# Performance work log

Measured on AMD Instinct MI355X. Metric: run time of the kernel, lower is better.

The kernel has to match this reference:

```python
import jax, jax.numpy as jnp
import numpy as np

DIM = 1024
NUM_HEADS = 16
HEAD_DIM = DIM // NUM_HEADS
SCALE = HEAD_DIM ** -0.5


def setup_inputs() -> dict:
    key = jax.random.key(0)
    k1, k2, k3 = jax.random.split(key, 3)
    B, S = 2, 2048
    x = jax.random.normal(k1, (B, S, DIM), dtype=jnp.float32)
    # nn.Linear(dim, 3*dim, bias=False): store as [in, out] for x @ W
    w_qkv = jax.random.normal(k2, (DIM, 3 * DIM), dtype=jnp.float32) * (DIM ** -0.5)
    w_out = jax.random.normal(k3, (DIM, DIM), dtype=jnp.float32) * (DIM ** -0.5)
    return {"x": x, "w_qkv": w_qkv, "w_out": w_out}


def reference(x, w_qkv, w_out):
    B, S, _ = x.shape
    qkv = x @ w_qkv                               # [B,S,3*D]
    q, k, v = jnp.split(qkv, 3, axis=-1)          # each [B,S,D]
    def heads(t):
        return t.reshape(B, S, NUM_HEADS, HEAD_DIM).transpose(0, 2, 1, 3)  # [B,H,S,d]
    q, k, v = heads(q), heads(k), heads(v)
    scores = jnp.einsum('bhqd,bhkd->bhqk', q, k) * SCALE   # [B,H,S,S]
    probs = jax.nn.softmax(scores, axis=-1)
    out = jnp.einsum('bhqk,bhkd->bhqd', probs, v)          # [B,H,S,d]
    out = out.transpose(0, 2, 1, 3).reshape(B, S, DIM)
    return out @ w_out
```

## Files before the change

kernel.cpp:

```cpp
#include <hip/hip_runtime.h>


typedef __bf16 bf16x8 __attribute__((ext_vector_type(8)));
typedef __bf16 bf16x4 __attribute__((ext_vector_type(4)));
typedef float floatx4 __attribute__((ext_vector_type(4)));

#define MFMA16(a, b, c) __builtin_amdgcn_mfma_f32_16x16x32_bf16((a), (b), (c), 0, 0, 0)

#if defined(__has_builtin)
#if __has_builtin(__builtin_amdgcn_exp2f)
#define EXP2F __builtin_amdgcn_exp2f
#endif
#endif
#ifndef EXP2F
#define EXP2F exp2f
#endif

__device__ __forceinline__ unsigned pk_bf16(float a, float b) {
  unsigned r;
  asm("v_cvt_pk_bf16_f32 %0, %1, %2" : "=v"(r) : "v"(a), "v"(b));
  return r;
}

__device__ __forceinline__ void gl_lds16(const void* g, void* l) {
  __builtin_amdgcn_global_load_lds((__attribute__((address_space(1))) void*)(g),
                                   (__attribute__((address_space(3))) void*)(l),
                                   16, 0, 0);
}

__global__ __launch_bounds__(256) void prep(const float* __restrict__ x,
                                            const float* __restrict__ w_qkv,
                                            const float* __restrict__ w_out,
                                            __bf16* __restrict__ xb,
                                            __bf16* __restrict__ wqkvt,
                                            __bf16* __restrict__ woutt) {
  __shared__ float tile[64][65];
  const int bid = blockIdx.x, t = threadIdx.x;
  if (bid < 4096) {
    int i = (bid * 256 + t) * 4;
    float4 v = *(const float4*)(x + i);
    bf16x4 o = { (__bf16)v.x, (__bf16)v.y, (__bf16)v.z, (__bf16)v.w };
    *(bf16x4*)(xb + i) = o;
    return;
  }
  const float* w;
  __bf16* wt;
  int K = 1024, N, k0, n0;
  if (bid < 4864) {
    int i = bid - 4096;
    w = w_qkv; wt = wqkvt; N = 3072; k0 = (i & 15) * 64; n0 = (i >> 4) * 64;
  } else {
    int i = bid - 4864;
    w = w_out; wt = woutt; N = 1024; k0 = (i & 15) * 64; n0 = (i >> 4) * 64;
  }
  for (int j = 0; j < 16; ++j) {
    int e = j * 256 + t, r = e >> 6, c = e & 63;
    tile[r][c] = w[(size_t)(k0 + r) * N + n0 + c];
  }
  __syncthreads();
  for (int j = 0; j < 16; ++j) {
    int e = j * 256 + t, r = e >> 6, c = e & 63;
    wt[(size_t)(n0 + r) * K + k0 + c] = (__bf16)tile[c][r];
  }
}

__global__ __launch_bounds__(256) void gemm_qkv(const __bf16* __restrict__ A,
                                                const __bf16* __restrict__ Bt,
                                                __bf16* __restrict__ qkb,
                                                __bf16* __restrict__ vt) {
  constexpr int K = 1024;
  constexpr float QSCALE = 0.18033688f;
  __shared__ __align__(16) __bf16 aS[128 * 32];
  __shared__ __align__(16) __bf16 bS[128 * 32];
  const int t = threadIdx.x;
  const int lane = t & 63, wave = t >> 6;
  const int l15 = lane & 15, quad = lane >> 4;
  const int wm = wave >> 1, wn = wave & 1;
  const int m0 = blockIdx.y * 128, n0 = blockIdx.x * 128;

  const floatx4 fzero = {0.f, 0.f, 0.f, 0.f};
  floatx4 acc[4][4];
  for (int mt = 0; mt < 4; ++mt)
    for (int nt = 0; nt < 4; ++nt) acc[mt][nt] = fzero;

  const int arow = t >> 2;
  const int ach = ((t & 3) ^ (arow & 3)) * 8;
  const __bf16* gA0 = A + (size_t)(m0 + arow) * K + ach;
  const __bf16* gA1 = gA0 + (size_t)64 * K;
  const __bf16* gB0 = Bt + (size_t)(n0 + arow) * K + ach;
  const __bf16* gB1 = gB0 + (size_t)64 * K;
  const int swz = (quad ^ (l15 & 3)) * 8;

  for (int k0 = 0; k0 < K; k0 += 32) {
    __syncthreads();
    gl_lds16(gA0 + k0, (char*)aS + t * 16);
    gl_lds16(gA1 + k0, (char*)aS + 4096 + t * 16);
    gl_lds16(gB0 + k0, (char*)bS + t * 16);
    gl_lds16(gB1 + k0, (char*)bS + 4096 + t * 16);
    __syncthreads();

    bf16x8 af[4], bfr[4];
    for (int mt = 0; mt < 4; ++mt)
      af[mt] = *(const bf16x8*)(aS + (wm * 64 + mt * 16 + l15) * 32 + swz);
    for (int nt = 0; nt < 4; ++nt)
      bfr[nt] = *(const bf16x8*)(bS + (wn * 64 + nt * 16 + l15) * 32 + swz);
    for (int mt = 0; mt < 4; ++mt)
      for (int nt = 0; nt < 4; ++nt)
        acc[mt][nt] = MFMA16(af[mt], bfr[nt], acc[mt][nt]);
  }

  for (int mt = 0; mt < 4; ++mt) {
    int row = m0 + wm * 64 + mt * 16 + quad * 4;
    for (int nt = 0; nt < 4; ++nt) {
      int col0 = n0 + wn * 64 + nt * 16;
      if (col0 >= 2048) {
        int dfull = col0 + l15 - 2048;
        int bh = ((row >> 11) << 4) + (dfull >> 6);
        int d = dfull & 63, s0 = row & 2047;
        bf16x4 pk = { (__bf16)acc[mt][nt][0], (__bf16)acc[mt][nt][1],
                      (__bf16)acc[mt][nt][2], (__bf16)acc[mt][nt][3] };
        *(bf16x4*)(vt + ((size_t)bh * 64 + d) * 2048 + s0) = pk;
      } else {
        float sc = (col0 < 1024) ? QSCALE : 1.0f;
        int col = col0 + l15;
        __bf16* cp = qkb + (size_t)row * 2048 + col;
        for (int r = 0; r < 4; ++r) cp[(size_t)r * 2048] = (__bf16)(acc[mt][nt][r] * sc);
      }
    }
  }
}

__global__ __launch_bounds__(256) void gemm_n64(const __bf16* __restrict__ A,
                                                const __bf16* __restrict__ Bt,
                                                float* __restrict__ C) {
  constexpr int K = 1024, N = 1024;
  __shared__ __align__(16) __bf16 aS[128 * 32];
  __shared__ __align__(16) __bf16 bS[64 * 32];
  const int t = threadIdx.x;
  const int lane = t & 63, wave = t >> 6;
  const int l15 = lane & 15, quad = lane >> 4;
  const int m0 = blockIdx.y * 128, n0 = blockIdx.x * 64;

  const floatx4 fzero = {0.f, 0.f, 0.f, 0.f};
  floatx4 acc[2][4];
  for (int mt = 0; mt < 2; ++mt)
    for (int nt = 0; nt < 4; ++nt) acc[mt][nt] = fzero;

  const int arow = t >> 2;
  const int ach = ((t & 3) ^ (arow & 3)) * 8;
  const __bf16* gA0 = A + (size_t)(m0 + arow) * K + ach;
  const __bf16* gA1 = gA0 + (size_t)64 * K;
  const __bf16* gB0 = Bt + (size_t)(n0 + arow) * K + ach;
  const int swz = (quad ^ (l15 & 3)) * 8;

  for (int k0 = 0; k0 < K; k0 += 32) {
    __syncthreads();
    gl_lds16(gA0 + k0, (char*)aS + t * 16);
    gl_lds16(gA1 + k0, (char*)aS + 4096 + t * 16);
    gl_lds16(gB0 + k0, (char*)bS + t * 16);
    __syncthreads();

    bf16x8 af[2], bfr[4];
    for (int mt = 0; mt < 2; ++mt)
      af[mt] = *(const bf16x8*)(aS + (wave * 32 + mt * 16 + l15) * 32 + swz);
    for (int nt = 0; nt < 4; ++nt)
      bfr[nt] = *(const bf16x8*)(bS + (nt * 16 + l15) * 32 + swz);
    for (int mt = 0; mt < 2; ++mt)
      for (int nt = 0; nt < 4; ++nt)
        acc[mt][nt] = MFMA16(af[mt], bfr[nt], acc[mt][nt]);
  }

  for (int mt = 0; mt < 2; ++mt) {
    int row = m0 + wave * 32 + mt * 16 + quad * 4;
    for (int nt = 0; nt < 4; ++nt) {
      int col = n0 + nt * 16 + l15;
      float* cp = C + (size_t)row * N + col;
      for (int r = 0; r < 4; ++r) cp[(size_t)r * N] = acc[mt][nt][r];
    }
  }
}

__global__ __launch_bounds__(256, 2) void flash_attn(const __bf16* __restrict__ qkb,
                                                     const __bf16* __restrict__ vt,
                                                     __bf16* __restrict__ out) {
  __shared__ __align__(16) __bf16 kS[2 * 64 * 64];
  __shared__ __align__(16) __bf16 vS[2 * 64 * 64];

  const int t = threadIdx.x;
  const int lane = t & 63, wave = t >> 6;
  const int l15 = lane & 15, quad = lane >> 4;
  const int id = blockIdx.x;
  const int xcd = id & 7, slot = id >> 3;
  const int bh = xcd * 4 + (slot >> 4), qb = slot & 15;
  const int b = bh >> 4, h = bh & 15;

  bf16x8 qf[2][2];
  for (int qt = 0; qt < 2; ++qt) {
    const __bf16* qp = qkb +
        (size_t)(b * 2048 + qb * 128 + wave * 32 + qt * 16 + l15) * 2048 + h * 64 + quad * 8;
    qf[qt][0] = *(const bf16x8*)qp;
    qf[qt][1] = *(const bf16x8*)(qp + 32);
  }

  bf16x8 onef;
  for (int j = 0; j < 8; ++j) onef[j] = (__bf16)1.0f;

  const floatx4 fzero = {0.f, 0.f, 0.f, 0.f};
  floatx4 oacc[2][4], lacc[2];
  for (int qt = 0; qt < 2; ++qt) {
    lacc[qt] = fzero;
    for (int dt = 0; dt < 4; ++dt) oacc[qt][dt] = fzero;
  }

  const int srow = t >> 3, schk = (t & 7) ^ (srow & 7);
  const __bf16* kg0 =
      qkb + (size_t)(b * 2048 + srow) * 2048 + 1024 + h * 64 + schk * 8;
  const __bf16* kg1 = kg0 + (size_t)32 * 2048;
  const __bf16* vg0 =
      vt + (size_t)bh * 64 * 2048 + (size_t)srow * 2048 + schk * 8;
  const __bf16* vg1 = vg0 + (size_t)32 * 2048;

  const int l7 = l15 & 7;

  bf16x8 kf[4][2];
  bf16x8 vfA[2][4], vfB[2][4];
  floatx4 saA[2][4], saB[2][4];

  auto stage = [&](int tile) {
    const size_t n1 = (size_t)tile * 64;
    const int oB = (tile & 1) * 8192;
    gl_lds16(kg0 + n1 * 2048, (char*)kS + oB + t * 16);
    gl_lds16(kg1 + n1 * 2048, (char*)kS + oB + 4096 + t * 16);
    gl_lds16(vg0 + n1, (char*)vS + oB + t * 16);
    gl_lds16(vg1 + n1, (char*)vS + oB + 4096 + t * 16);
  };

  auto loadKV = [&](int buf, bf16x8 (&vf)[2][4]) {
    const __bf16* kC = kS + buf * 4096;
    const __bf16* vC = vS + buf * 4096;
    for (int nt = 0; nt < 4; ++nt)
      for (int ks = 0; ks < 2; ++ks)
        kf[nt][ks] = *(const bf16x8*)(kC + (nt * 16 + l15) * 64 +
                                      ((ks * 4 + quad) ^ l7) * 8);
    for (int ks = 0; ks < 2; ++ks)
      for (int dt = 0; dt < 4; ++dt)
        vf[ks][dt] = *(const bf16x8*)(vC + (dt * 16 + l15) * 64 +
                                      ((ks * 4 + quad) ^ l7) * 8);
  };

  auto qk = [&](floatx4 (&sa)[2][4]) {
    __builtin_amdgcn_s_setprio(1);
    for (int qt = 0; qt < 2; ++qt)
      for (int nt = 0; nt < 4; ++nt) {
        floatx4 a = fzero;
        a = MFMA16(kf[nt][0], qf[qt][0], a);
        a = MFMA16(kf[nt][1], qf[qt][1], a);
        sa[qt][nt] = a;
      }
    __builtin_amdgcn_s_setprio(0);
  };

  auto smpv = [&](floatx4 (&sa)[2][4], bf16x8 (&vf)[2][4]) {
    for (int qt = 0; qt < 2; ++qt) {
      bf16x8 pa[2];
      for (int ks = 0; ks < 2; ++ks) {
        const int n0 = 2 * ks, n1 = 2 * ks + 1;
        float e00 = EXP2F(sa[qt][n0][0]), e01 = EXP2F(sa[qt][n0][1]);
        float e02 = EXP2F(sa[qt][n0][2]), e03 = EXP2F(sa[qt][n0][3]);
        float e10 = EXP2F(sa[qt][n1][0]), e11 = EXP2F(sa[qt][n1][1]);
        float e12 = EXP2F(sa[qt][n1][2]), e13 = EXP2F(sa[qt][n1][3]);
        unsigned x0 = pk_bf16(e00, e01), x1 = pk_bf16(e02, e03);
        unsigned y0 = pk_bf16(e10, e11), y1 = pk_bf16(e12, e13);
        unsigned d0 = x0, d2 = y0;
        asm("v_permlane32_swap_b32 %0, %1" : "+v"(d0), "+v"(d2));
        asm("v_permlane16_swap_b32 %0, %1" : "+v"(d0), "+v"(d2));
        unsigned d1 = x1, d3 = y1;
        asm("v_permlane32_swap_b32 %0, %1" : "+v"(d1), "+v"(d3));
        asm("v_permlane16_swap_b32 %0, %1" : "+v"(d1), "+v"(d3));
        union { unsigned u[4]; bf16x8 v8; } pu;
        pu.u[0] = d0; pu.u[1] = d1; pu.u[2] = d2; pu.u[3] = d3;
        pa[ks] = pu.v8;
      }
      __builtin_amdgcn_s_setprio(1);
      for (int ks = 0; ks < 2; ++ks) {
        for (int dt = 0; dt < 4; ++dt)
          oacc[qt][dt] = MFMA16(pa[ks], vf[ks][dt], oacc[qt][dt]);
        lacc[qt] = MFMA16(pa[ks], onef, lacc[qt]);
      }
      __builtin_amdgcn_s_setprio(0);
    }
  };

  stage(0);
  __syncthreads();
  stage(1);
  loadKV(0, vfA);
  qk(saA);

  for (int nb = 1; nb < 31; nb += 2) {
    __syncthreads();
    stage(nb + 1);
    loadKV(1, vfB);
    smpv(saA, vfA);
    qk(saB);
    __syncthreads();
    stage(nb + 2);
    loadKV(0, vfA);
    smpv(saB, vfB);
    qk(saA);
  }

  __syncthreads();
  loadKV(1, vfB);
  smpv(saA, vfA);
  qk(saB);
  smpv(saB, vfB);

  for (int qt = 0; qt < 2; ++qt) {
    float inv[4];
    for (int r = 0; r < 4; ++r) inv[r] = 1.f / lacc[qt][r];
    __bf16* ob = out +
        (size_t)(b * 2048 + qb * 128 + wave * 32 + qt * 16 + quad * 4) * 1024 + h * 64;
    for (int dt = 0; dt < 4; ++dt)
      for (int r = 0; r < 4; ++r)
        ob[(size_t)r * 1024 + dt * 16 + l15] = (__bf16)(oacc[qt][dt][r] * inv[r]);
  }
}

extern "C" void kernel_launch(void* const* d_in, const int* in_sizes, int n_in,
                              void* d_out, int out_size, void* d_ws, size_t ws_size,
                              hipStream_t stream) {
  const float* x = (const float*)d_in[0];
  const float* w_qkv = (const float*)d_in[1];
  const float* w_out = (const float*)d_in[2];
  float* out = (float*)d_out;

  char* ws = (char*)d_ws;
  __bf16* xb = (__bf16*)(ws);
  __bf16* wqkvt = (__bf16*)(ws + ((size_t)8 << 20));
  __bf16* qkb = (__bf16*)(ws + ((size_t)16 << 20));
  __bf16* vtg = (__bf16*)(ws + ((size_t)32 << 20));
  __bf16* aout = (__bf16*)(ws + ((size_t)40 << 20));
  __bf16* woutt = (__bf16*)(ws + ((size_t)48 << 20));

  prep<<<5120, 256, 0, stream>>>(x, w_qkv, w_out, xb, wqkvt, woutt);
  gemm_qkv<<<dim3(24, 32), 256, 0, stream>>>(xb, wqkvt, qkb, vtg);
  flash_attn<<<512, 256, 0, stream>>>(qkb, vtg, aout);
  gemm_n64<<<dim3(16, 32), 256, 0, stream>>>(aout, woutt, out);
}
```

Measured before the change: 172.9 us.

## Rewrite QKV GEMM with 256x256 tiles, double-buffered LDS, and split-phase MFMA pipeline

The QKV projection GEMM moves from 128x128 tiles with 256 threads and a single LDS buffer to 256x256 tiles with 512 threads, a BK of 64, and double-buffered LDS. Global-to-LDS loads for the next k-step are issued while MFMAs run on the current buffer. Explicit vmcnt/lgkmcnt waits, s_setprio and sched barriers control the interleaving. This is meant to hide memory latency and improve data reuse, at the cost of 128KB of LDS per block, much higher register pressure (32 accumulators per thread), and only 192 blocks, which could leave some CUs idle.

Result: slower. 176.8 us (+2.2%).

```diff
diff --git a/kernel.cpp b/kernel.cpp
--- a/kernel.cpp
+++ b/kernel.cpp
@@ -64,70 +64,146 @@
   }
 }
 
-__global__ __launch_bounds__(256) void gemm_qkv(const __bf16* __restrict__ A,
-                                                const __bf16* __restrict__ Bt,
-                                                __bf16* __restrict__ qkb,
-                                                __bf16* __restrict__ vt) {
+__global__ __launch_bounds__(512, 2) void gemm_qkv(const __bf16* __restrict__ A,
+                                                   const __bf16* __restrict__ Bt,
+                                                   __bf16* __restrict__ qkb,
+                                                   __bf16* __restrict__ vt) {
   constexpr int K = 1024;
   constexpr float QSCALE = 0.18033688f;
-  __shared__ __align__(16) __bf16 aS[128 * 32];
-  __shared__ __align__(16) __bf16 bS[128 * 32];
+  __shared__ __align__(16) __bf16 aL[2][2][128 * 64];
+  __shared__ __align__(16) __bf16 bL[2][2][128 * 64];
   const int t = threadIdx.x;
   const int lane = t & 63, wave = t >> 6;
-  const int l15 = lane & 15, quad = lane >> 4;
-  const int wm = wave >> 1, wn = wave & 1;
-  const int m0 = blockIdx.y * 128, n0 = blockIdx.x * 128;
+  const int l15 = lane & 15, quad = lane >> 4, l7 = l15 & 7;
+  const int wr = wave >> 2, wc = wave & 3;
+  const int m0 = blockIdx.y * 256, n0 = blockIdx.x * 256;
 
   const floatx4 fzero = {0.f, 0.f, 0.f, 0.f};
-  floatx4 acc[4][4];
-  for (int mt = 0; mt < 4; ++mt)
-    for (int nt = 0; nt < 4; ++nt) acc[mt][nt] = fzero;
-
-  const int arow = t >> 2;
-  const int ach = ((t & 3) ^ (arow & 3)) * 8;
-  const __bf16* gA0 = A + (size_t)(m0 + arow) * K + ach;
-  const __bf16* gA1 = gA0 + (size_t)64 * K;
-  const __bf16* gB0 = Bt + (size_t)(n0 + arow) * K + ach;
-  const __bf16* gB1 = gB0 + (size_t)64 * K;
-  const int swz = (quad ^ (l15 & 3)) * 8;
-
-  for (int k0 = 0; k0 < K; k0 += 32) {
-    __syncthreads();
-    gl_lds16(gA0 + k0, (char*)aS + t * 16);
-    gl_lds16(gA1 + k0, (char*)aS + 4096 + t * 16);
-    gl_lds16(gB0 + k0, (char*)bS + t * 16);
-    gl_lds16(gB1 + k0, (char*)bS + 4096 + t * 16);
-    __syncthreads();
-
-    bf16x8 af[4], bfr[4];
-    for (int mt = 0; mt < 4; ++mt)
-      af[mt] = *(const bf16x8*)(aS + (wm * 64 + mt * 16 + l15) * 32 + swz);
-    for (int nt = 0; nt < 4; ++nt)
-      bfr[nt] = *(const bf16x8*)(bS + (wn * 64 + nt * 16 + l15) * 32 + swz);
-    for (int mt = 0; mt < 4; ++mt)
-      for (int nt = 0; nt < 4; ++nt)
-        acc[mt][nt] = MFMA16(af[mt], bfr[nt], acc[mt][nt]);
-  }
-
-  for (int mt = 0; mt < 4; ++mt) {
-    int row = m0 + wm * 64 + mt * 16 + quad * 4;
-    for (int nt = 0; nt < 4; ++nt) {
-      int col0 = n0 + wn * 64 + nt * 16;
+  floatx4 acc[8][4];
+#pragma unroll
+  for (int i = 0; i < 8; ++i)
+#pragma unroll
+    for (int j = 0; j < 4; ++j) acc[i][j] = fzero;
+
+  const int r0 = t >> 3;
+  const int c8 = ((t & 7) ^ (r0 & 7)) * 8;
+  const __bf16* gA = A + (size_t)(m0 + r0) * K + c8;
+  const __bf16* gB = Bt + (size_t)(n0 + r0) * K + c8;
+
+#define STAGE_A(buf, kofs)                                        \
+  do {                                                            \
+    char* d0 = (char*)aL[buf][0] + t * 16;                        \
+    char* d1 = (char*)aL[buf][1] + t * 16;                        \
+    gl_lds16(gA + (kofs), d0);                                    \
+    gl_lds16(gA + (size_t)64 * K + (kofs), d0 + 8192);            \
+    gl_lds16(gA + (size_t)128 * K + (kofs), d1);                  \
+    gl_lds16(gA + (size_t)192 * K + (kofs), d1 + 8192);           \
+  } while (0)
+
+#define STAGE_B(buf, kofs)                                        \
+  do {                                                            \
+    char* d0 = (char*)bL[buf][0] + t * 16;                        \
+    char* d1 = (char*)bL[buf][1] + t * 16;                        \
+    gl_lds16(gB + (kofs), d0);                                    \
+    gl_lds16(gB + (size_t)64 * K + (kofs), d0 + 8192);            \
+    gl_lds16(gB + (size_t)128 * K + (kofs), d1);                  \
+    gl_lds16(gB + (size_t)192 * K + (kofs), d1 + 8192);           \
+  } while (0)
+
+  bf16x8 af[4][2], bf[4][2];
+#define LOAD_B(buf)                                                       \
+  do {                                                                    \
+    const __bf16* base = bL[buf][wc >> 1] + (wc & 1) * 64 * 64;           \
+    _Pragma("unroll") for (int nf = 0; nf < 4; ++nf)                      \
+        _Pragma("unroll") for (int kk = 0; kk < 2; ++kk)                  \
+            bf[nf][kk] = *(const bf16x8*)(base + (nf * 16 + l15) * 64 +   \
+                                          ((kk * 4 + quad) ^ l7) * 8);    \
+  } while (0)
+
+#define LOAD_A(buf, mh)                                                   \
+  do {                                                                    \
+    const __bf16* base = aL[buf][wr] + (mh) * 64 * 64;                    \
+    _Pragma("unroll") for (int mf = 0; mf < 4; ++mf)                      \
+        _Pragma("unroll") for (int kk = 0; kk < 2; ++kk)                  \
+            af[mf][kk] = *(const bf16x8*)(base + (mf * 16 + l15) * 64 +   \
+                                          ((kk * 4 + quad) ^ l7) * 8);    \
+  } while (0)
+
+#define MFMA_PH(mh)                                                       \
+  do {                                                                    \
+    __builtin_amdgcn_s_setprio(1);                                        \
+    _Pragma("unroll") for (int mf = 0; mf < 4; ++mf)                      \
+        _Pragma("unroll") for (int nf = 0; nf < 4; ++nf) {                \
+      floatx4 c = acc[(mh) * 4 + mf][nf];                                 \
+      c = MFMA16(af[mf][0], bf[nf][0], c);                                \
+      c = MFMA16(af[mf][1], bf[nf][1], c);                                \
+      acc[(mh) * 4 + mf][nf] = c;                                         \
+    }                                                                     \
+    __builtin_amdgcn_s_setprio(0);                                        \
+  } while (0)
+
+#define VMCNT4 asm volatile("s_waitcnt vmcnt(4)" ::: "memory")
+#define VMCNT0 asm volatile("s_waitcnt vmcnt(0)" ::: "memory")
+#define LGKM0 asm volatile("s_waitcnt lgkmcnt(0)" ::: "memory")
+#define BAR asm volatile("s_barrier" ::: "memory")
+#define SCHED0 __builtin_amdgcn_sched_barrier(0)
+
+  STAGE_A(0, 0);
+  STAGE_B(0, 0);
+
+  for (int j = 0; j < 15; ++j) {
+    const int cb = j & 1, nb = cb ^ 1;
+    const int kn = (j + 1) * 64;
+    STAGE_A(nb, kn);
+    VMCNT4;
+    BAR;
+    LOAD_B(cb);
+    LOAD_A(cb, 0);
+    LGKM0; SCHED0;
+    MFMA_PH(0);
+    STAGE_B(nb, kn);
+    LOAD_A(cb, 1);
+    LGKM0; SCHED0;
+    MFMA_PH(1);
+    BAR;
+  }
+  VMCNT0;
+  BAR;
+  LOAD_B(1);
+  LOAD_A(1, 0);
+  LGKM0; SCHED0;
+  MFMA_PH(0);
+  LOAD_A(1, 1);
+  LGKM0; SCHED0;
+  MFMA_PH(1);
+
+#pragma unroll
+  for (int mf8 = 0; mf8 < 8; ++mf8) {
+    int row = m0 + wr * 128 + mf8 * 16 + quad * 4;
+#pragma unroll
+    for (int nf = 0; nf < 4; ++nf) {
+      int col0 = n0 + wc * 64 + nf * 16;
       if (col0 >= 2048) {
         int dfull = col0 + l15 - 2048;
         int bh = ((row >> 11) << 4) + (dfull >> 6);
         int d = dfull & 63, s0 = row & 2047;
-        bf16x4 pk = { (__bf16)acc[mt][nt][0], (__bf16)acc[mt][nt][1],
-                      (__bf16)acc[mt][nt][2], (__bf16)acc[mt][nt][3] };
+        bf16x4 pk = { (__bf16)acc[mf8][nf][0], (__bf16)acc[mf8][nf][1],
+                      (__bf16)acc[mf8][nf][2], (__bf16)acc[mf8][nf][3] };
         *(bf16x4*)(vt + ((size_t)bh * 64 + d) * 2048 + s0) = pk;
       } else {
         float sc = (col0 < 1024) ? QSCALE : 1.0f;
         int col = col0 + l15;
         __bf16* cp = qkb + (size_t)row * 2048 + col;
-        for (int r = 0; r < 4; ++r) cp[(size_t)r * 2048] = (__bf16)(acc[mt][nt][r] * sc);
+#pragma unroll
+        for (int r = 0; r < 4; ++r) cp[(size_t)r * 2048] = (__bf16)(acc[mf8][nf][r] * sc);
       }
     }
   }
+#undef STAGE_A
+#undef STAGE_B
+#undef LOAD_A
+#undef LOAD_B
+#undef MFMA_PH
 }
 
 __global__ __launch_bounds__(256) void gemm_n64(const __bf16* __restrict__ A,
@@ -344,7 +420,7 @@
   __bf16* woutt = (__bf16*)(ws + ((size_t)48 << 20));
 
   prep<<<5120, 256, 0, stream>>>(x, w_qkv, w_out, xb, wqkvt, woutt);
-  gemm_qkv<<<dim3(24, 32), 256, 0, stream>>>(xb, wqkvt, qkb, vtg);
+  gemm_qkv<<<dim3(12, 16), 512, 0, stream>>>(xb, wqkvt, qkb, vtg);
   flash_attn<<<512, 256, 0, stream>>>(qkb, vtg, aout);
   gemm_n64<<<dim3(16, 32), 256, 0, stream>>>(aout, woutt, out);
 }
```

## Double-buffer GEMM LDS tiles with BK=64 and async prefetch pipeline

Applied to the files above, without the earlier changes.

Both projection GEMMs now stage 64-wide K tiles into double-buffered LDS, issuing the next tile's global-to-LDS loads before computing on the current one. Explicit vmcnt waits and barriers replace the two syncthreads per step. The loads use an 8-way XOR swizzle, and MFMA sections get raised wave priority. This is meant to hide global load latency and halve barrier count, at the cost of more LDS per block (64KB/48KB), which may limit occupancy despite launch_bounds(256,2).

Measured after the change: 173.7 us. No clear change (+0.4%).

```diff
diff --git a/kernel.cpp b/kernel.cpp
--- a/kernel.cpp
+++ b/kernel.cpp
@@ -27,6 +27,11 @@
                                    (__attribute__((address_space(3))) void*)(l),
                                    16, 0, 0);
 }
+
+#define VMCNT(n) asm volatile("s_waitcnt vmcnt(" #n ")" ::: "memory")
+#define LGKM0 asm volatile("s_waitcnt lgkmcnt(0)" ::: "memory")
+#define SBAR __builtin_amdgcn_s_barrier()
+#define SCHED0 __builtin_amdgcn_sched_barrier(0)
 
 __global__ __launch_bounds__(256) void prep(const float* __restrict__ x,
                                             const float* __restrict__ w_qkv,
@@ -64,118 +69,203 @@
   }
 }
 
-__global__ __launch_bounds__(256) void gemm_qkv(const __bf16* __restrict__ A,
-                                                const __bf16* __restrict__ Bt,
-                                                __bf16* __restrict__ qkb,
-                                                __bf16* __restrict__ vt) {
+__global__ __launch_bounds__(256, 2) void gemm_qkv(const __bf16* __restrict__ A,
+                                                   const __bf16* __restrict__ Bt,
+                                                   __bf16* __restrict__ qkb,
+                                                   __bf16* __restrict__ vt) {
   constexpr int K = 1024;
   constexpr float QSCALE = 0.18033688f;
-  __shared__ __align__(16) __bf16 aS[128 * 32];
-  __shared__ __align__(16) __bf16 bS[128 * 32];
+  __shared__ __align__(16) __bf16 aL[2][128 * 64];
+  __shared__ __align__(16) __bf16 bL[2][128 * 64];
   const int t = threadIdx.x;
   const int lane = t & 63, wave = t >> 6;
-  const int l15 = lane & 15, quad = lane >> 4;
+  const int l15 = lane & 15, quad = lane >> 4, l7 = l15 & 7;
   const int wm = wave >> 1, wn = wave & 1;
   const int m0 = blockIdx.y * 128, n0 = blockIdx.x * 128;
 
   const floatx4 fzero = {0.f, 0.f, 0.f, 0.f};
   floatx4 acc[4][4];
-  for (int mt = 0; mt < 4; ++mt)
-    for (int nt = 0; nt < 4; ++nt) acc[mt][nt] = fzero;
-
-  const int arow = t >> 2;
-  const int ach = ((t & 3) ^ (arow & 3)) * 8;
-  const __bf16* gA0 = A + (size_t)(m0 + arow) * K + ach;
-  const __bf16* gA1 = gA0 + (size_t)64 * K;
-  const __bf16* gB0 = Bt + (size_t)(n0 + arow) * K + ach;
-  const __bf16* gB1 = gB0 + (size_t)64 * K;
-  const int swz = (quad ^ (l15 & 3)) * 8;
-
-  for (int k0 = 0; k0 < K; k0 += 32) {
-    __syncthreads();
-    gl_lds16(gA0 + k0, (char*)aS + t * 16);
-    gl_lds16(gA1 + k0, (char*)aS + 4096 + t * 16);
-    gl_lds16(gB0 + k0, (char*)bS + t * 16);
-    gl_lds16(gB1 + k0, (char*)bS + 4096 + t * 16);
-    __syncthreads();
-
-    bf16x8 af[4], bfr[4];
-    for (int mt = 0; mt < 4; ++mt)
-      af[mt] = *(const bf16x8*)(aS + (wm * 64 + mt * 16 + l15) * 32 + swz);
-    for (int nt = 0; nt < 4; ++nt)
-      bfr[nt] = *(const bf16x8*)(bS + (wn * 64 + nt * 16 + l15) * 32 + swz);
-    for (int mt = 0; mt < 4; ++mt)
-      for (int nt = 0; nt < 4; ++nt)
-        acc[mt][nt] = MFMA16(af[mt], bfr[nt], acc[mt][nt]);
-  }
-
-  for (int mt = 0; mt < 4; ++mt) {
-    int row = m0 + wm * 64 + mt * 16 + quad * 4;
-    for (int nt = 0; nt < 4; ++nt) {
-      int col0 = n0 + wn * 64 + nt * 16;
+#pragma unroll
+  for (int i = 0; i < 4; ++i)
+#pragma unroll
+    for (int j = 0; j < 4; ++j) acc[i][j] = fzero;
+
+  const int r0 = t >> 3;
+  const int c8 = ((t & 7) ^ (r0 & 7)) * 8;
+  const __bf16* gA = A + (size_t)(m0 + r0) * K + c8;
+  const __bf16* gB = Bt + (size_t)(n0 + r0) * K + c8;
+
+  auto stageAB = [&](int buf, int kofs) {
+    char* da = (char*)aL[buf] + t * 16;
+    char* db = (char*)bL[buf] + t * 16;
+#pragma unroll
+    for (int r = 0; r < 4; ++r) {
+      gl_lds16(gA + (size_t)(32 * r) * K + kofs, da + r * 4096);
+      gl_lds16(gB + (size_t)(32 * r) * K + kofs, db + r * 4096);
+    }
+  };
+
+  bf16x8 af[4][2], bfr[4][2];
+  auto loadAB = [&](int buf) {
+#pragma unroll
+    for (int mf = 0; mf < 4; ++mf)
+#pragma unroll
+      for (int kk = 0; kk < 2; ++kk)
+        af[mf][kk] = *(const bf16x8*)(aL[buf] + (wm * 64 + mf * 16 + l15) * 64 +
+                                      ((kk * 4 + quad) ^ l7) * 8);
+#pragma unroll
+    for (int nf = 0; nf < 4; ++nf)
+#pragma unroll
+      for (int kk = 0; kk < 2; ++kk)
+        bfr[nf][kk] = *(const bf16x8*)(bL[buf] + (wn * 64 + nf * 16 + l15) * 64 +
+                                       ((kk * 4 + quad) ^ l7) * 8);
+  };
+
+  auto mfmaAll = [&]() {
+    __builtin_amdgcn_s_setprio(1);
+#pragma unroll
+    for (int mf = 0; mf < 4; ++mf)
+#pragma unroll
+      for (int nf = 0; nf < 4; ++nf) {
+        floatx4 c = acc[mf][nf];
+        c = MFMA16(af[mf][0], bfr[nf][0], c);
+        c = MFMA16(af[mf][1], bfr[nf][1], c);
+        acc[mf][nf] = c;
+      }
+    __builtin_amdgcn_s_setprio(0);
+  };
+
+  stageAB(0, 0);
+  for (int j = 0; j < 15; ++j) {
+    const int cb = j & 1;
+    stageAB(cb ^ 1, (j + 1) * 64);
+    VMCNT(8);
+    SBAR;
+    loadAB(cb);
+    LGKM0; SCHED0;
+    mfmaAll();
+    SBAR;
+  }
+  VMCNT(0);
+  SBAR;
+  loadAB(1);
+  LGKM0; SCHED0;
+  mfmaAll();
+
+#pragma unroll
+  for (int mf = 0; mf < 4; ++mf) {
+    int row = m0 + wm * 64 + mf * 16 + quad * 4;
+#pragma unroll
+    for (int nf = 0; nf < 4; ++nf) {
+      int col0 = n0 + wn * 64 + nf * 16;
       if (col0 >= 2048) {
         int dfull = col0 + l15 - 2048;
         int bh = ((row >> 11) << 4) + (dfull >> 6);
         int d = dfull & 63, s0 = row & 2047;
-        bf16x4 pk = { (__bf16)acc[mt][nt][0], (__bf16)acc[mt][nt][1],
-                      (__bf16)acc[mt][nt][2], (__bf16)acc[mt][nt][3] };
+        bf16x4 pk = { (__bf16)acc[mf][nf][0], (__bf16)acc[mf][nf][1],
+                      (__bf16)acc[mf][nf][2], (__bf16)acc[mf][nf][3] };
         *(bf16x4*)(vt + ((size_t)bh * 64 + d) * 2048 + s0) = pk;
       } else {
         float sc = (col0 < 1024) ? QSCALE : 1.0f;
         int col = col0 + l15;
         __bf16* cp = qkb + (size_t)row * 2048 + col;
-        for (int r = 0; r < 4; ++r) cp[(size_t)r * 2048] = (__bf16)(acc[mt][nt][r] * sc);
+#pragma unroll
+        for (int r = 0; r < 4; ++r) cp[(size_t)r * 2048] = (__bf16)(acc[mf][nf][r] * sc);
       }
     }
   }
 }
 
-__global__ __launch_bounds__(256) void gemm_n64(const __bf16* __restrict__ A,
-                                                const __bf16* __restrict__ Bt,
-                                                float* __restrict__ C) {
+__global__ __launch_bounds__(256, 2) void gemm_n64(const __bf16* __restrict__ A,
+                                                   const __bf16* __restrict__ Bt,
+                                                   float* __restrict__ C) {
   constexpr int K = 1024, N = 1024;
-  __shared__ __align__(16) __bf16 aS[128 * 32];
-  __shared__ __align__(16) __bf16 bS[64 * 32];
+  __shared__ __align__(16) __bf16 aL[2][128 * 64];
+  __shared__ __align__(16) __bf16 bL[2][64 * 64];
   const int t = threadIdx.x;
   const int lane = t & 63, wave = t >> 6;
-  const int l15 = lane & 15, quad = lane >> 4;
+  const int l15 = lane & 15, quad = lane >> 4, l7 = l15 & 7;
   const int m0 = blockIdx.y * 128, n0 = blockIdx.x * 64;
 
   const floatx4 fzero = {0.f, 0.f, 0.f, 0.f};
   floatx4 acc[2][4];
-  for (int mt = 0; mt < 2; ++mt)
-    for (int nt = 0; nt < 4; ++nt) acc[mt][nt] = fzero;
-
-  const int arow = t >> 2;
-  const int ach = ((t & 3) ^ (arow & 3)) * 8;
-  const __bf16* gA0 = A + (size_t)(m0 + arow) * K + ach;
-  const __bf16* gA1 = gA0 + (size_t)64 * K;
-  const __bf16* gB0 = Bt + (size_t)(n0 + arow) * K + ach;
-  const int swz = (quad ^ (l15 & 3)) * 8;
-
-  for (int k0 = 0; k0 < K; k0 += 32) {
-    __syncthreads();
-    gl_lds16(gA0 + k0, (char*)aS + t * 16);
-    gl_lds16(gA1 + k0, (char*)aS + 4096 + t * 16);
-    gl_lds16(gB0 + k0, (char*)bS + t * 16);
-    __syncthreads();
-
-    bf16x8 af[2], bfr[4];
-    for (int mt = 0; mt < 2; ++mt)
-      af[mt] = *(const bf16x8*)(aS + (wave * 32 + mt * 16 + l15) * 32 + swz);
-    for (int nt = 0; nt < 4; ++nt)
-      bfr[nt] = *(const bf16x8*)(bS + (nt * 16 + l15) * 32 + swz);
-    for (int mt = 0; mt < 2; ++mt)
-      for (int nt = 0; nt < 4; ++nt)
-        acc[mt][nt] = MFMA16(af[mt], bfr[nt], acc[mt][nt]);
-  }
-
-  for (int mt = 0; mt < 2; ++mt) {
-    int row = m0 + wave * 32 + mt * 16 + quad * 4;
-    for (int nt = 0; nt < 4; ++nt) {
-      int col = n0 + nt * 16 + l15;
+#pragma unroll
+  for (int i = 0; i < 2; ++i)
+#pragma unroll
+    for (int j = 0; j < 4; ++j) acc[i][j] = fzero;
+
+  const int r0 = t >> 3;
+  const int c8 = ((t & 7) ^ (r0 & 7)) * 8;
+  const __bf16* gA = A + (size_t)(m0 + r0) * K + c8;
+  const __bf16* gB = Bt + (size_t)(n0 + r0) * K + c8;
+
+  auto stageAB = [&](int buf, int kofs) {
+    char* da = (char*)aL[buf] + t * 16;
+    char* db = (char*)bL[buf] + t * 16;
+#pragma unroll
+    for (int r = 0; r < 4; ++r)
+      gl_lds16(gA + (size_t)(32 * r) * K + kofs, da + r * 4096);
+#pragma unroll
+    for (int r = 0; r < 2; ++r)
+      gl_lds16(gB + (size_t)(32 * r) * K + kofs, db + r * 4096);
+  };
+
+  bf16x8 af[2][2], bfr[4][2];
+  auto loadAB = [&](int buf) {
+#pragma unroll
+    for (int mf = 0; mf < 2; ++mf)
+#pragma unroll
+      for (int kk = 0; kk < 2; ++kk)
+        af[mf][kk] = *(const bf16x8*)(aL[buf] + (wave * 32 + mf * 16 + l15) * 64 +
+                                      ((kk * 4 + quad) ^ l7) * 8);
+#pragma unroll
+    for (int nf = 0; nf < 4; ++nf)
+#pragma unroll
+      for (int kk = 0; kk < 2; ++kk)
+        bfr[nf][kk] = *(const bf16x8*)(bL[buf] + (nf * 16 + l15) * 64 +
+                                       ((kk * 4 + quad) ^ l7) * 8);
+  };
+
+  auto mfmaAll = [&]() {
+    __builtin_amdgcn_s_setprio(1);
+#pragma unroll
+    for (int mf = 0; mf < 2; ++mf)
+#pragma unroll
+      for (int nf = 0; nf < 4; ++nf) {
+        floatx4 c = acc[mf][nf];
+        c = MFMA16(af[mf][0], bfr[nf][0], c);
+        c = MFMA16(af[mf][1], bfr[nf][1], c);
+        acc[mf][nf] = c;
+      }
+    __builtin_amdgcn_s_setprio(0);
+  };
+
+  stageAB(0, 0);
+  for (int j = 0; j < 15; ++j) {
+    const int cb = j & 1;
+    stageAB(cb ^ 1, (j + 1) * 64);
+    VMCNT(6);
+    SBAR;
+    loadAB(cb);
+    LGKM0; SCHED0;
+    mfmaAll();
+    SBAR;
+  }
+  VMCNT(0);
+  SBAR;
+  loadAB(1);
+  LGKM0; SCHED0;
+  mfmaAll();
+
+#pragma unroll
+  for (int mf = 0; mf < 2; ++mf) {
+    int row = m0 + wave * 32 + mf * 16 + quad * 4;
+#pragma unroll
+    for (int nf = 0; nf < 4; ++nf) {
+      int col = n0 + nf * 16 + l15;
       float* cp = C + (size_t)row * N + col;
-      for (int r = 0; r < 4; ++r) cp[(size_t)r * N] = acc[mt][nt][r];
+#pragma unroll
+      for (int r = 0; r < 4; ++r) cp[(size_t)r * N] = acc[mf][nf][r];
     }
   }
 }
```
